# Kernel optimization log

Hardware: AMD Instinct MI355X
Metric: run time of the kernel (lower is better)

The kernel has to match this reference:

```python
import jax, jax.numpy as jnp
import numpy as np

N, E, CS = 8, 256, 8
L2, M2 = 2048, 1024
L1 = M2 * CS            # 8192 tokens at depth-1
M1 = 4096
LLAST = M1 * CS         # 32768 tokens at last layer
S = L2 + L1 + LLAST     # 43008
NUM_VOCAB = 16
RES = 64


def _mixed_values(key, n, L, M):
    # values in {1,3}, with exactly M positions per row set to the 'mixed' token 2
    k1, k2 = jax.random.split(key)
    base = jax.random.randint(k1, (n, L), 0, 2) * 2 + 1
    perms = jax.vmap(lambda k: jax.random.permutation(k, L))(jax.random.split(k2, n))
    mask = jnp.zeros((n, L), bool).at[jnp.arange(n)[:, None], perms[:, :M]].set(True)
    return jnp.where(mask, 2, base).astype(jnp.int32)


def setup_inputs() -> dict:
    key = jax.random.key(0)
    ks = jax.random.split(key, 16)
    v2 = _mixed_values(ks[0], N, L2, M2)
    v1 = _mixed_values(ks[1], N, L1, M1)
    vl = jax.random.randint(ks[2], (N, LLAST), 1, 4).astype(jnp.int32)
    value = jnp.concatenate([v2, v1, vl], axis=1)
    depth = jnp.concatenate([
        jnp.full((N, L2), 4, jnp.int32),
        jnp.full((N, L1), 5, jnp.int32),
        jnp.full((N, LLAST), 6, jnp.int32)], axis=1)
    pos = jax.random.randint(ks[3], (N, S, 3), 0, RES).astype(jnp.int32)
    x = jax.random.normal(ks[4], (N, L2 // CS, E), jnp.float32)
    s = 0.02
    return {
        'x': x, 'value': value, 'depth': depth, 'pos': pos,
        'W2': jax.random.normal(ks[5], (E, E, CS), jnp.float32) * s,
        'b2': jax.random.normal(ks[6], (E,), jnp.float32) * s,
        'W1': jax.random.normal(ks[7], (E, E, CS), jnp.float32) * s,
        'b1': jax.random.normal(ks[8], (E,), jnp.float32) * s,
        'W0': jax.random.normal(ks[9], (E, E, CS), jnp.float32) * s,
        'b0': jax.random.normal(ks[10], (E,), jnp.float32) * s,
        'emb': jax.random.normal(ks[11], (3, RES, E), jnp.float32) * s,
        'lin_w': jax.random.normal(ks[12], (E, NUM_VOCAB + 1), jnp.float32) * s,
        'lin_b': jax.random.normal(ks[13], (NUM_VOCAB + 1,), jnp.float32) * s,
    }


def _deconv(h, W, b):
    # ConvTranspose1d with kernel_size == stride == CS: each input token emits CS outputs
    n, t, e = h.shape
    cs = W.shape[2]
    return jnp.einsum('nti,iok->ntko', h, W).reshape(n, t * cs, e) + b


def _compact(y, mask, M):
    # per-row: rows of y where mask, packed to the front (stable), zero padded to M rows
    T = y.shape[1]
    if mask.shape[1] < T:
        mask = jnp.pad(mask, ((0, 0), (0, T - mask.shape[1])))
    else:
        mask = mask[:, :T]
    order = jnp.argsort(jnp.where(mask, 0, 1), axis=1, stable=True)
    g = jnp.take_along_axis(y, order[:, :M, None], axis=1)
    keep = jnp.arange(M)[None, :] < jnp.sum(mask, axis=1)[:, None]
    return jnp.where(keep[:, :, None], g, 0.0)


def reference(x, value, depth, pos, W2, b2, W1, b1, W0, b0, emb, lin_w, lin_b):
    max_depth = int(jnp.max(depth))
    len_1 = jnp.sum(depth == max_depth - 1, axis=1)
    len_2 = jnp.sum(depth == max_depth - 2, axis=1)
    L1_ = int(jnp.max(len_1)); L2_ = int(jnp.max(len_2))
    j2 = jnp.arange(L2_); j1 = jnp.arange(L1_)
    val_2 = jnp.where(j2[None, :] < len_2[:, None], value[:, :L2_], 0)
    idx1 = jnp.clip(len_2[:, None] + j1[None, :], 0, value.shape[1] - 1)
    val_1 = jnp.where(j1[None, :] < len_1[:, None], jnp.take_along_axis(value, idx1, axis=1), 0)
    mix_1 = jnp.sum(val_1 == 2, axis=1); mix_2 = jnp.sum(val_2 == 2, axis=1)
    M1_ = int(jnp.max(mix_1)); M2_ = int(jnp.max(mix_2))

    y_2 = _deconv(x, W2, b2)                 # [N, T''*cs, E]
    x_1 = _compact(y_2, val_2 == 2, M2_)     # gather mixed depth-2 positions
    y_1 = _deconv(x_1, W1, b1)
    x_0 = _compact(y_1, val_1 == 2, M1_)     # gather mixed depth-1 positions
    y_0 = _deconv(x_0, W0, b0)               # [N, M1_*cs, E]

    len_last = int(jnp.sum(depth[0] == max_depth))  # uniform across batch (torch slicing requires it)
    p = pos[:, -len_last:]                   # [N, len_last, 3]
    enc = emb[0][p[..., 0]] + emb[1][p[..., 1]] + emb[2][p[..., 2]]
    y_0 = y_0 + enc
    return y_0 @ lin_w + lin_b
```

## Files before the change

### kernel.cpp

```cpp
#include <hip/hip_runtime.h>
#include <cstdint>
#include <cstddef>

#define SEQ     43008
#define LASTOFF 10240
#define NV      17

typedef __bf16 bf16x8 __attribute__((ext_vector_type(8)));
typedef float  f32x4  __attribute__((ext_vector_type(4)));

typedef __attribute__((address_space(1))) const void gv_t;
typedef __attribute__((address_space(3))) void       lv_t;

__device__ __forceinline__ ushort f2bf(float f) {
    union { float f; unsigned u; } x; x.f = f;
    unsigned r = x.u + 0x7FFFu + ((x.u >> 16) & 1u);
    return (ushort)(r >> 16);
}
__device__ __forceinline__ float bf2f(ushort h) {
    union { unsigned u; float f; } x; x.u = ((unsigned)h) << 16;
    return x.f;
}

__device__ __forceinline__ void stage_tile_w(char* ldsbase, const ushort* src,
                                             int row0, int k0, int nch, int wv,
                                             int nwv, int lane)
{
    int sub  = lane >> 3;
    int col8 = (lane & 7) ^ sub;
    const ushort* g0 = src + (size_t)(row0 + sub) * 256 + k0 + (col8 << 3);
    for (int ch = wv; ch < nch; ch += nwv) {
        const ushort* g = g0 + ((size_t)(ch << 3)) * 256;
        __builtin_amdgcn_global_load_lds((gv_t*)g, (lv_t*)(ldsbase + (ch << 10)), 16, 0, 0);
    }
}

__device__ __forceinline__ bf16x8 frag64(const char* lds, int row, int kk, int lane) {
    int r = row + (lane & 15);
    int byte = (r << 7) + ((kk + ((lane >> 4) << 3)) << 1);
    byte ^= (r & 7) << 4;
    return *(const bf16x8*)(lds + byte);
}

__global__ __launch_bounds__(256) void prep_main(
    const float* __restrict__ x, const float* __restrict__ W2,
    const float* __restrict__ W1, const float* __restrict__ W0,
    const float* __restrict__ lin_w, const int* __restrict__ value,
    const float* __restrict__ emb, const float* __restrict__ b0,
    const float* __restrict__ lin_b,
    ushort* __restrict__ xb, ushort* __restrict__ WbT,
    ushort* __restrict__ W1n, int* __restrict__ dest2,
    int* __restrict__ packT, int* __restrict__ cnt1,
    float* __restrict__ embLp)
{
    __shared__ __align__(16) char sm[33792];
    const int b = blockIdx.x;
    const int tid = threadIdx.x;

    if (b < 192) {
        int s   = b >> 6;
        int rem = b & 63;
        int i0  = (rem >> 3) << 5;
        int o0  = (rem & 7) << 5;
        const float* W = (s == 0) ? W2 : ((s == 1) ? W1 : W0);
        float* tl = (float*)sm;
        #pragma unroll
        for (int q = 0; q < 8; ++q) {
            int fid = (q << 8) + tid;
            int ri  = fid >> 6;
            int f   = (fid & 63) << 2;
            float4 v = *(const float4*)(W + (size_t)(i0 + ri) * 2048 + o0 * 8 + f);
            int ol = f >> 3;
            int c0 = f & 7;
            tl[((c0 + 0) * 32 + ol) * 33 + ri] = v.x;
            tl[((c0 + 1) * 32 + ol) * 33 + ri] = v.y;
            tl[((c0 + 2) * 32 + ol) * 33 + ri] = v.z;
            tl[((c0 + 3) * 32 + ol) * 33 + ri] = v.w;
        }
        __syncthreads();
        int seg = tid & 3;
        if (s == 1) {
            #pragma unroll
            for (int it = 0; it < 4; ++it) {
                int rk = (it << 6) + (tid >> 2);
                int c = rk >> 5, ii = rk & 31;
                ushort v8[8];
                #pragma unroll
                for (int u = 0; u < 8; ++u)
                    v8[u] = f2bf(tl[(c * 32 + (seg << 3) + u) * 33 + ii]);
                *(int4*)(W1n + (c << 16) + (i0 + ii) * 256 + o0 + (seg << 3)) =
                    *(const int4*)v8;
            }
        } else {
            #pragma unroll
            for (int it = 0; it < 4; ++it) {
                int rk = (it << 6) + (tid >> 2);
                int j  = ((rk >> 5) << 8) + o0 + (rk & 31);
                ushort v8[8];
                #pragma unroll
                for (int u = 0; u < 8; ++u)
                    v8[u] = f2bf(tl[rk * 33 + (seg << 3) + u]);
                *(int4*)(WbT + ((size_t)s << 19) + ((size_t)j << 8) + i0 + (seg << 3)) =
                    *(const int4*)v8;
            }
        }
    } else if (b < 448) {
        int i8 = (((b - 192) << 8) + tid) << 3;
        float4 a  = *(const float4*)(x + i8);
        float4 bb = *(const float4*)(x + i8 + 4);
        ushort v[8] = { f2bf(a.x), f2bf(a.y), f2bf(a.z), f2bf(a.w),
                        f2bf(bb.x), f2bf(bb.y), f2bf(bb.z), f2bf(bb.w) };
        *(int4*)(xb + i8) = *(const int4*)v;
    } else if (b < 456) {
        int n    = b - 448;
        int base = n * SEQ;
        int* dst = dest2 + n * 2048;
        int cnt = 0;
        int vloc[8];
        #pragma unroll
        for (int i = 0; i < 8; ++i) {
            vloc[i] = value[base + tid * 8 + i];
            cnt += (vloc[i] == 2);
        }
        int* s = (int*)sm;
        s[tid] = cnt;
        __syncthreads();
        for (int off = 1; off < 256; off <<= 1) {
            int v = (tid >= off) ? s[tid - off] : 0;
            __syncthreads();
            s[tid] += v;
            __syncthreads();
        }
        int run = s[tid] - cnt;
        #pragma unroll
        for (int i = 0; i < 8; ++i) {
            int d = -1;
            if (vloc[i] == 2 && run < 1024) { d = run; ++run; }
            dst[tid * 8 + i] = d;
        }
    } else if (b < 464) {
        int n    = b - 456;
        int base = n * SEQ + 2048;
        int (*s8)[8] = (int(*)[8])sm;
        int cnt8[8] = {0,0,0,0,0,0,0,0};
        int vloc[32];
        #pragma unroll
        for (int i = 0; i < 32; ++i) {
            vloc[i] = value[base + tid * 32 + i];
            cnt8[i & 7] += (vloc[i] == 2);
        }
        #pragma unroll
        for (int k = 0; k < 8; ++k) s8[tid][k] = cnt8[k];
        __syncthreads();
        for (int off = 1; off < 256; off <<= 1) {
            int v[8];
            #pragma unroll
            for (int k = 0; k < 8; ++k) v[k] = (tid >= off) ? s8[tid - off][k] : 0;
            __syncthreads();
            #pragma unroll
            for (int k = 0; k < 8; ++k) s8[tid][k] += v[k];
            __syncthreads();
        }
        int runK[8], runTot = 0;
        #pragma unroll
        for (int k = 0; k < 8; ++k) { runK[k] = s8[tid][k] - cnt8[k]; runTot += runK[k]; }
        #pragma unroll
        for (int i = 0; i < 32; ++i) {
            if (vloc[i] == 2) {
                int k  = i & 7;
                int tp = (tid * 32 + i) >> 3;
                packT[(((n << 3) + k) << 10) + runK[k]] = (runTot << 16) | tp;
                runK[k]++; runTot++;
            }
        }
        if (tid < 8) cnt1[(n << 3) + tid] = s8[255][tid];
    } else {
        int idx = b - 464;
        int jd  = idx >> 6;
        int p   = idx & 63;
        float* er = (float*)sm;
        float* ps = er + 256;
        float e = emb[jd * 16384 + p * 256 + tid];
        if (jd == 0) e += b0[tid];
        er[tid] = e;
        __syncthreads();
        if (tid < 136) {
            int v = tid >> 3, part = tid & 7;
            const float* lw = lin_w + v;
            float s = 0.f;
            int o0 = part << 5;
            #pragma unroll 8
            for (int o = o0; o < o0 + 32; ++o)
                s = fmaf(er[o], lw[o * NV], s);
            ps[tid] = s;
        }
        __syncthreads();
        if (tid < 20) {
            float acc = 0.f;
            if (tid < NV) {
                #pragma unroll
                for (int q = 0; q < 8; ++q) acc += ps[tid * 8 + q];
                if (jd == 0) acc += lin_b[tid];
            }
            embLp[jd * 1280 + p * 20 + tid] = acc;
        }
    }
}

__global__ __launch_bounds__(256) void prep_g2(
    const ushort* __restrict__ Wb0T, const float* __restrict__ lin_w,
    ushort* __restrict__ Gt,
    const ushort* __restrict__ A, const ushort* __restrict__ BT,
    const float* __restrict__ bias, const int* __restrict__ dest,
    ushort* __restrict__ Xout)
{
    __shared__ __align__(16) char smem[65536];
    const int tid = threadIdx.x;

    if (blockIdx.x < 144) {
        int col = blockIdx.x;
        if (col >= 136) { Gt[col * 256 + tid] = 0; return; }
        int c = (col * 964) >> 14;
        int v = col - c * 17;
        float* lw = (float*)smem;
        lw[tid] = lin_w[tid * NV + v];
        __syncthreads();
        const ushort* wrow = Wb0T + ((size_t)c << 16) + tid;
        float acc = 0.f;
        #pragma unroll 4
        for (int q = 0; q < 256; ++q)
            acc = fmaf(lw[q], bf2f(wrow[q << 8]), acc);
        Gt[col * 256 + tid] = f2bf(acc);
        return;
    }

    const int bx   = blockIdx.x - 144;
    const int lane = tid & 63, wv = tid >> 6;
    const int r0 = (bx & 15) << 7;
    const int c0 = (bx >> 4) << 7;
    const int wm = (wv >> 1) << 6;
    const int wn = (wv & 1) << 6;

    f32x4 acc[4][4] = {};

    stage_tile_w(smem,         A,  r0, 0, 16, wv, 4, lane);
    stage_tile_w(smem + 16384, BT, c0, 0, 16, wv, 4, lane);
    __syncthreads();

    for (int kt = 0; kt < 4; ++kt) {
        char* cb = smem + ((kt & 1) << 15);
        if (kt < 3) {
            char* nb = smem + (((kt + 1) & 1) << 15);
            int k0n = (kt + 1) << 6;
            stage_tile_w(nb,         A,  r0, k0n, 16, wv, 4, lane);
            stage_tile_w(nb + 16384, BT, c0, k0n, 16, wv, 4, lane);
        }
        #pragma unroll
        for (int ks = 0; ks < 2; ++ks) {
            int kk = ks << 5;
            bf16x8 af[4], bfr[4];
            #pragma unroll
            for (int i = 0; i < 4; ++i) af[i]  = frag64(cb, wm + i * 16, kk, lane);
            #pragma unroll
            for (int i = 0; i < 4; ++i) bfr[i] = frag64(cb + 16384, wn + i * 16, kk, lane);
            #pragma unroll
            for (int mi = 0; mi < 4; ++mi)
                #pragma unroll
                for (int ni = 0; ni < 4; ++ni)
                    acc[mi][ni] = __builtin_amdgcn_mfma_f32_16x16x32_bf16(
                        af[mi], bfr[ni], acc[mi][ni], 0, 0, 0);
        }
        __syncthreads();
    }

    const int obase = c0 & 255;
    const int cdx   = c0 >> 8;
    float bv[4];
    #pragma unroll
    for (int ni = 0; ni < 4; ++ni)
        bv[ni] = bias[obase + wn + ni * 16 + (lane & 15)];

    ushort* Cs = (ushort*)smem;
    #pragma unroll
    for (int mi = 0; mi < 4; ++mi)
        #pragma unroll
        for (int ni = 0; ni < 4; ++ni)
            #pragma unroll
            for (int r = 0; r < 4; ++r) {
                int row = wm + mi * 16 + ((lane >> 4) << 2) + r;
                int col = wn + ni * 16 + (lane & 15);
                Cs[row * 136 + col] = f2bf(acc[mi][ni][r] + bv[ni]);
            }
    __syncthreads();

    for (int p = 0; p < 8; ++p) {
        int row = p * 16 + (tid >> 4);
        int gr  = r0 + row;
        int n   = gr >> 8, t = gr & 255;
        int d   = dest[n * 2048 + t * 8 + cdx];
        if (d >= 0) {
            int4 v = *(const int4*)&Cs[row * 136 + ((tid & 15) << 3)];
            *(int4*)&Xout[(((size_t)n * 1024 + d) << 8) + obase + ((tid & 15) << 3)] = v;
        }
    }
}

__global__ __launch_bounds__(256) void prep_H(
    const ushort* __restrict__ Gt, const ushort* __restrict__ W1n,
    const float* __restrict__ b1, ushort* __restrict__ Hf,
    float* __restrict__ K1f)
{
    __shared__ __align__(16) char smem[38912];
    const int tid = threadIdx.x, lane = tid & 63, wv = tid >> 6;
    const int cp = blockIdx.y, fb = blockIdx.x;

    if (cp == 8) {
        if (fb != 0) return;
        float* bs = (float*)smem;
        bs[tid] = b1[tid];
        __syncthreads();
        if (tid < 144) {
            const ushort* gr = Gt + tid * 256;
            float acc = 0.f;
            #pragma unroll 8
            for (int o = 0; o < 256; ++o)
                acc = fmaf(bs[o], bf2f(gr[o]), acc);
            K1f[tid] = acc;
        }
        return;
    }

    const ushort* Wb = W1n + (cp << 16);
    f32x4 acc[3][4] = {};

    for (int kt = 0; kt < 4; ++kt) {
        int k0 = kt << 6;
        stage_tile_w(smem,        Gt, fb * 48, k0, 6,  wv, 4, lane);
        stage_tile_w(smem + 6144, Wb, 0,       k0, 32, wv, 4, lane);
        __syncthreads();
        #pragma unroll
        for (int ks = 0; ks < 2; ++ks) {
            int kk = ks << 5;
            bf16x8 af[3], bfr[4];
            #pragma unroll
            for (int mi = 0; mi < 3; ++mi) af[mi]  = frag64(smem, mi * 16, kk, lane);
            #pragma unroll
            for (int ni = 0; ni < 4; ++ni) bfr[ni] = frag64(smem + 6144, (wv << 6) + ni * 16, kk, lane);
            #pragma unroll
            for (int mi = 0; mi < 3; ++mi)
                #pragma unroll
                for (int ni = 0; ni < 4; ++ni)
                    acc[mi][ni] = __builtin_amdgcn_mfma_f32_16x16x32_bf16(
                        af[mi], bfr[ni], acc[mi][ni], 0, 0, 0);
        }
        __syncthreads();
    }

    #pragma unroll
    for (int mi = 0; mi < 3; ++mi)
        #pragma unroll
        for (int ni = 0; ni < 4; ++ni)
            #pragma unroll
            for (int r = 0; r < 4; ++r) {
                int f = fb * 48 + mi * 16 + ((lane >> 4) << 2) + r;
                int i = (wv << 6) + ni * 16 + (lane & 15);
                Hf[cp * 36864 + f * 256 + i] = f2bf(acc[mi][ni][r]);
            }
}

__global__ __launch_bounds__(256) void fused_out(
    const ushort* __restrict__ X1, const ushort* __restrict__ Hf,
    const float* __restrict__ embLp, const float* __restrict__ K1f,
    const int* __restrict__ packT, const int* __restrict__ cnt1,
    const int* __restrict__ pos, float* __restrict__ out)
{
    extern __shared__ __align__(16) char smem[];

    const int tid  = threadIdx.x;
    const int lane = tid & 63, wv = tid >> 6;
    const int bb = blockIdx.x;
    const int n  = bb >> 3, cp = bb & 7;
    const int t0 = blockIdx.y << 6;
    const int cnt = cnt1[bb];
    if (t0 >= cnt) return;
    const int cntL = min(64, cnt - t0);

    const int sub  = lane >> 3;
    const int col8 = (lane & 7) ^ sub;
    const int* pbase = packT + (bb << 10);
    int Ta = pbase[t0 + (wv << 3) + sub] & 1023;
    int Tb = pbase[t0 + ((wv + 4) << 3) + sub] & 1023;
    const ushort* ga0 = X1 + ((size_t)((n << 10) + Ta) << 8) + (col8 << 3);
    const ushort* gb0 = X1 + ((size_t)((n << 10) + Tb) << 8) + (col8 << 3);

    float* embLs = (float*)(smem + 53248);
    for (int i = tid; i < 3840; i += 256) embLs[i] = embLp[i];
    float* K1s = (float*)(smem + 68608);
    if (tid < 144) K1s[tid] = K1f[tid];
    int* Ds = (int*)(smem + 69184);
    if (tid < 64) Ds[tid] = (pbase[t0 + tid] >> 16) & 4095;

    const ushort* Hb = Hf + cp * 36864;

    __builtin_amdgcn_global_load_lds((gv_t*)ga0, (lv_t*)(smem + (wv << 10)), 16, 0, 0);
    __builtin_amdgcn_global_load_lds((gv_t*)gb0, (lv_t*)(smem + ((wv + 4) << 10)), 16, 0, 0);
    stage_tile_w(smem + 8192, Hb, 0, 0, 18, wv, 4, lane);
    __syncthreads();

    f32x4 acc[9] = {};
    for (int kt = 0; kt < 4; ++kt) {
        char* cb = smem + (kt & 1) * 26624;
        if (kt < 3) {
            char* nb = smem + ((kt + 1) & 1) * 26624;
            int k0n = (kt + 1) << 6;
            __builtin_amdgcn_global_load_lds((gv_t*)(ga0 + k0n), (lv_t*)(nb + (wv << 10)), 16, 0, 0);
            __builtin_amdgcn_global_load_lds((gv_t*)(gb0 + k0n), (lv_t*)(nb + ((wv + 4) << 10)), 16, 0, 0);
            stage_tile_w(nb + 8192, Hb, 0, k0n, 18, wv, 4, lane);
        }
        #pragma unroll
        for (int ks = 0; ks < 2; ++ks) {
            int kk = ks << 5;
            bf16x8 af = frag64(cb, wv << 4, kk, lane);
            #pragma unroll
            for (int ni = 0; ni < 9; ++ni) {
                bf16x8 bfr = frag64(cb + 8192, ni << 4, kk, lane);
                acc[ni] = __builtin_amdgcn_mfma_f32_16x16x32_bf16(af, bfr, acc[ni], 0, 0, 0);
            }
        }
        __syncthreads();
    }

    float* Cs = (float*)smem;
    #pragma unroll
    for (int ni = 0; ni < 9; ++ni) {
        int col = (ni << 4) + (lane & 15);
        if (col < 136) {
            #pragma unroll
            for (int r = 0; r < 4; ++r) {
                int row = (wv << 4) + ((lane >> 4) << 2) + r;
                Cs[row * 136 + col] = acc[ni][r];
            }
        }
    }
    __syncthreads();

    #pragma unroll
    for (int rr = 0; rr < 2; ++rr) {
        int rl = tid * 2 + rr;
        int r  = rl >> 3, c = rl & 7;
        int prow = n * SEQ + LASTOFF + (Ds[r] << 3) + c;
        const int* pp = pos + 3 * prow;
        const float* e0 = embLs +        pp[0] * 20;
        const float* e1 = embLs + 1280 + pp[1] * 20;
        const float* e2 = embLs + 2560 + pp[2] * 20;
        const float* k1 = K1s + c * 17;
        float* cr = Cs + rl * 17;
        #pragma unroll
        for (int v4 = 0; v4 < 16; v4 += 4) {
            float4 a = *(const float4*)(e0 + v4);
            float4 bq = *(const float4*)(e1 + v4);
            float4 cq = *(const float4*)(e2 + v4);
            cr[v4 + 0] += a.x + bq.x + cq.x + k1[v4 + 0];
            cr[v4 + 1] += a.y + bq.y + cq.y + k1[v4 + 1];
            cr[v4 + 2] += a.z + bq.z + cq.z + k1[v4 + 2];
            cr[v4 + 3] += a.w + bq.w + cq.w + k1[v4 + 3];
        }
        cr[16] += e0[16] + e1[16] + e2[16] + k1[16];
    }
    __syncthreads();

    for (int i4 = tid; i4 < 2176; i4 += 256) {
        int r  = (i4 * 1928) >> 16;
        int fo = i4 - r * 34;
        if (r < cntL) {
            *(float4*)(out + ((size_t)((n << 12) + Ds[r])) * 136 + (fo << 2)) =
                *(const float4*)(Cs + r * 136 + (fo << 2));
        }
    }
}

extern "C" void kernel_launch(void* const* d_in, const int* in_sizes, int n_in,
                              void* d_out, int out_size, void* d_ws, size_t ws_size,
                              hipStream_t stream)
{
    (void)in_sizes; (void)n_in; (void)out_size; (void)ws_size;
    const float* x     = (const float*)d_in[0];
    const int*   value = (const int*)d_in[1];
    const int*   pos   = (const int*)d_in[3];
    const float* W2    = (const float*)d_in[4];
    const float* b2    = (const float*)d_in[5];
    const float* W1    = (const float*)d_in[6];
    const float* b1    = (const float*)d_in[7];
    const float* W0    = (const float*)d_in[8];
    const float* b0    = (const float*)d_in[9];
    const float* emb   = (const float*)d_in[10];
    const float* lin_w = (const float*)d_in[11];
    const float* lin_b = (const float*)d_in[12];
    float* out = (float*)d_out;

    char* ws = (char*)d_ws;
    ushort* WbT   = (ushort*)(ws);
    ushort* Wb2T  = WbT;
    ushort* Wb0T  = WbT + 1048576;
    ushort* W1n   = (ushort*)(ws + 3145728);
    ushort* xb    = (ushort*)(ws + 4194304);
    int*    dest2 = (int*)   (ws + 5242880);
    int*    cnt1  = (int*)   (ws + 5308416);
    int*    packT = (int*)   (ws + 5308672);
    ushort* x1b   = (ushort*)(ws + 5570816);
    ushort* Gt    = (ushort*)(ws + 9765120);
    float*  embLp = (float*) (ws + 9838848);
    ushort* Hf    = (ushort*)(ws + 9854208);
    float*  K1f   = (float*) (ws + 10444032);

    prep_main<<<656, 256, 0, stream>>>(x, W2, W1, W0, lin_w, value,
                                       emb, b0, lin_b,
                                       xb, WbT, W1n, dest2, packT, cnt1, embLp);
    prep_g2<<<400, 256, 0, stream>>>(Wb0T, lin_w, Gt, xb, Wb2T, b2, dest2, x1b);
    prep_H<<<dim3(3, 9), 256, 0, stream>>>(Gt, W1n, b1, Hf, K1f);

    fused_out<<<dim3(64, 16), 256, 69632, stream>>>(x1b, Hf, embLp, K1f,
                                                    packT, cnt1, pos, out);
}
```

Baseline: 62.88 us.

## Fuse Gt and H precomputation into the depth-2 deconv kernel

Merges prep_g2 and prep_H into one kernel g2h. Its first 256 blocks run the depth-2 GEMM and scatter, and 64 extra blocks each compute the Gt slice (W0 folded with lin_w) for one channel group and then run the H GEMM against W1 straight from shared memory. K1f is computed by a reduction in the cp==0 blocks. This removes one kernel launch and the Gt round trip through global memory. In exchange, each (cp,cf) block recomputes its Gt slice redundantly, eight times in total, and the small blocks may form a tail behind the large GEMM blocks.

```diff
diff --git a/kernel.cpp b/kernel.cpp
--- a/kernel.cpp
+++ b/kernel.cpp
@@ -207,165 +207,182 @@
     }
 }
 
-__global__ __launch_bounds__(256) void prep_g2(
-    const ushort* __restrict__ Wb0T, const float* __restrict__ lin_w,
-    ushort* __restrict__ Gt,
+__global__ __launch_bounds__(256) void g2h(
     const ushort* __restrict__ A, const ushort* __restrict__ BT,
     const float* __restrict__ bias, const int* __restrict__ dest,
-    ushort* __restrict__ Xout)
+    ushort* __restrict__ Xout,
+    const ushort* __restrict__ Wb0T, const float* __restrict__ lin_w,
+    const ushort* __restrict__ W1n, const float* __restrict__ b1,
+    ushort* __restrict__ Hf, float* __restrict__ K1f)
 {
-    __shared__ __align__(16) char smem[65536];
+    extern __shared__ __align__(16) char smem[];
     const int tid = threadIdx.x;
 
-    if (blockIdx.x < 144) {
-        int col = blockIdx.x;
-        if (col >= 136) { Gt[col * 256 + tid] = 0; return; }
-        int c = (col * 964) >> 14;
-        int v = col - c * 17;
-        float* lw = (float*)smem;
-        lw[tid] = lin_w[tid * NV + v];
-        __syncthreads();
-        const ushort* wrow = Wb0T + ((size_t)c << 16) + tid;
-        float acc = 0.f;
-        #pragma unroll 4
-        for (int q = 0; q < 256; ++q)
-            acc = fmaf(lw[q], bf2f(wrow[q << 8]), acc);
-        Gt[col * 256 + tid] = f2bf(acc);
+    if (blockIdx.x < 256) {
+        const int lane = tid & 63, wv = tid >> 6;
+        const int bx = blockIdx.x;
+        const int r0 = (bx & 15) << 7;
+        const int c0 = (bx >> 4) << 7;
+        const int wm = (wv >> 1) << 6;
+        const int wn = (wv & 1) << 6;
+
+        f32x4 acc[4][4] = {};
+
+        stage_tile_w(smem,         A,  r0, 0, 16, wv, 4, lane);
+        stage_tile_w(smem + 16384, BT, c0, 0, 16, wv, 4, lane);
+        __syncthreads();
+
+        for (int kt = 0; kt < 4; ++kt) {
+            char* cb = smem + ((kt & 1) << 15);
+            if (kt < 3) {
+                char* nb = smem + (((kt + 1) & 1) << 15);
+                int k0n = (kt + 1) << 6;
+                stage_tile_w(nb,         A,  r0, k0n, 16, wv, 4, lane);
+                stage_tile_w(nb + 16384, BT, c0, k0n, 16, wv, 4, lane);
+            }
+            #pragma unroll
+            for (int ks = 0; ks < 2; ++ks) {
+                int kk = ks << 5;
+                bf16x8 af[4], bfr[4];
+                #pragma unroll
+                for (int i = 0; i < 4; ++i) af[i]  = frag64(cb, wm + i * 16, kk, lane);
+                #pragma unroll
+                for (int i = 0; i < 4; ++i) bfr[i] = frag64(cb + 16384, wn + i * 16, kk, lane);
+                #pragma unroll
+                for (int mi = 0; mi < 4; ++mi)
+                    #pragma unroll
+                    for (int ni = 0; ni < 4; ++ni)
+                        acc[mi][ni] = __builtin_amdgcn_mfma_f32_16x16x32_bf16(
+                            af[mi], bfr[ni], acc[mi][ni], 0, 0, 0);
+            }
+            __syncthreads();
+        }
+
+        const int obase = c0 & 255;
+        const int cdx   = c0 >> 8;
+        float bv[4];
+        #pragma unroll
+        for (int ni = 0; ni < 4; ++ni)
+            bv[ni] = bias[obase + wn + ni * 16 + (lane & 15)];
+
+        ushort* Cs = (ushort*)smem;
+        #pragma unroll
+        for (int mi = 0; mi < 4; ++mi)
+            #pragma unroll
+            for (int ni = 0; ni < 4; ++ni)
+                #pragma unroll
+                for (int r = 0; r < 4; ++r) {
+                    int row = wm + mi * 16 + ((lane >> 4) << 2) + r;
+                    int col = wn + ni * 16 + (lane & 15);
+                    Cs[row * 136 + col] = f2bf(acc[mi][ni][r] + bv[ni]);
+                }
+        __syncthreads();
+
+        for (int p = 0; p < 8; ++p) {
+            int row = p * 16 + (tid >> 4);
+            int gr  = r0 + row;
+            int n   = gr >> 8, t = gr & 255;
+            int d   = dest[n * 2048 + t * 8 + cdx];
+            if (d >= 0) {
+                int4 v = *(const int4*)&Cs[row * 136 + ((tid & 15) << 3)];
+                *(int4*)&Xout[(((size_t)n * 1024 + d) << 8) + obase + ((tid & 15) << 3)] = v;
+            }
+        }
         return;
     }
 
-    const int bx   = blockIdx.x - 144;
+    const int idx = blockIdx.x - 256;
+    const int cp  = idx >> 3, cf = idx & 7;
     const int lane = tid & 63, wv = tid >> 6;
-    const int r0 = (bx & 15) << 7;
-    const int c0 = (bx >> 4) << 7;
-    const int wm = (wv >> 1) << 6;
-    const int wn = (wv & 1) << 6;
-
-    f32x4 acc[4][4] = {};
-
-    stage_tile_w(smem,         A,  r0, 0, 16, wv, 4, lane);
-    stage_tile_w(smem + 16384, BT, c0, 0, 16, wv, 4, lane);
-    __syncthreads();
-
+
+    float* lwS = (float*)smem;
+    float* b1S = (float*)(smem + 17408);
+    for (int j = tid; j < 4352; j += 256) {
+        int v = j >> 8, q = j & 255;
+        lwS[j] = lin_w[q * NV + v];
+    }
+    b1S[tid] = b1[tid];
+    __syncthreads();
+
+    float gv[17];
+    #pragma unroll
+    for (int v = 0; v < 17; ++v) gv[v] = 0.f;
+    const ushort* wb = Wb0T + ((size_t)cf << 16) + tid;
+    for (int q = 0; q < 256; ++q) {
+        float w = bf2f(wb[q << 8]);
+        #pragma unroll
+        for (int v = 0; v < 17; ++v)
+            gv[v] = fmaf(w, lwS[(v << 8) + q], gv[v]);
+    }
+
+    float* Kr = (float*)(smem + 20480);
+    {
+        float bo = b1S[tid];
+        #pragma unroll
+        for (int v = 0; v < 17; ++v) Kr[(v << 8) + tid] = gv[v] * bo;
+    }
+    __syncthreads();
+    if (cp == 0) {
+        for (int s = 128; s >= 1; s >>= 1) {
+            for (int v = 0; v < 17; ++v)
+                if (tid < s) Kr[(v << 8) + tid] += Kr[(v << 8) + tid + s];
+            __syncthreads();
+        }
+        if (tid < 17) K1f[cf * 17 + tid] = Kr[tid << 8];
+        if (cf == 7 && tid >= 136 && tid < 144) K1f[tid] = 0.f;
+    }
+    __syncthreads();
+
+    ushort* Gs = (ushort*)smem;
+    for (int j = tid; j < 4096; j += 256) ((int*)Gs)[j] = 0;
+    __syncthreads();
+    {
+        int kt = tid >> 6, kloc = tid & 63;
+        #pragma unroll
+        for (int v = 0; v < 17; ++v) {
+            int byte = (v << 7) + (kloc << 1);
+            byte ^= (v & 7) << 4;
+            *(ushort*)((char*)Gs + (kt << 12) + byte) = f2bf(gv[v]);
+        }
+    }
+    __syncthreads();
+
+    char* Bs = smem + 16384;
+    const ushort* Wb1 = W1n + ((size_t)cp << 16);
+    f32x4 hacc[2][16] = {};
     for (int kt = 0; kt < 4; ++kt) {
-        char* cb = smem + ((kt & 1) << 15);
-        if (kt < 3) {
-            char* nb = smem + (((kt + 1) & 1) << 15);
-            int k0n = (kt + 1) << 6;
-            stage_tile_w(nb,         A,  r0, k0n, 16, wv, 4, lane);
-            stage_tile_w(nb + 16384, BT, c0, k0n, 16, wv, 4, lane);
-        }
+        stage_tile_w(Bs, Wb1, 0, kt << 6, 32, wv, 4, lane);
+        __syncthreads();
         #pragma unroll
         for (int ks = 0; ks < 2; ++ks) {
             int kk = ks << 5;
-            bf16x8 af[4], bfr[4];
-            #pragma unroll
-            for (int i = 0; i < 4; ++i) af[i]  = frag64(cb, wm + i * 16, kk, lane);
-            #pragma unroll
-            for (int i = 0; i < 4; ++i) bfr[i] = frag64(cb + 16384, wn + i * 16, kk, lane);
-            #pragma unroll
-            for (int mi = 0; mi < 4; ++mi)
-                #pragma unroll
-                for (int ni = 0; ni < 4; ++ni)
-                    acc[mi][ni] = __builtin_amdgcn_mfma_f32_16x16x32_bf16(
-                        af[mi], bfr[ni], acc[mi][ni], 0, 0, 0);
-        }
-        __syncthreads();
-    }
-
-    const int obase = c0 & 255;
-    const int cdx   = c0 >> 8;
-    float bv[4];
+            bf16x8 af0 = frag64((char*)Gs + (kt << 12), 0,  kk, lane);
+            bf16x8 af1 = frag64((char*)Gs + (kt << 12), 16, kk, lane);
+            #pragma unroll
+            for (int ni = 0; ni < 16; ++ni) {
+                bf16x8 bfr = frag64(Bs, ni << 4, kk, lane);
+                hacc[0][ni] = __builtin_amdgcn_mfma_f32_16x16x32_bf16(af0, bfr, hacc[0][ni], 0, 0, 0);
+                hacc[1][ni] = __builtin_amdgcn_mfma_f32_16x16x32_bf16(af1, bfr, hacc[1][ni], 0, 0, 0);
+            }
+        }
+        __syncthreads();
+    }
+
     #pragma unroll
-    for (int ni = 0; ni < 4; ++ni)
-        bv[ni] = bias[obase + wn + ni * 16 + (lane & 15)];
-
-    ushort* Cs = (ushort*)smem;
-    #pragma unroll
-    for (int mi = 0; mi < 4; ++mi)
-        #pragma unroll
-        for (int ni = 0; ni < 4; ++ni)
+    for (int mi = 0; mi < 2; ++mi)
+        #pragma unroll
+        for (int ni = 0; ni < 16; ++ni)
             #pragma unroll
             for (int r = 0; r < 4; ++r) {
-                int row = wm + mi * 16 + ((lane >> 4) << 2) + r;
-                int col = wn + ni * 16 + (lane & 15);
-                Cs[row * 136 + col] = f2bf(acc[mi][ni][r] + bv[ni]);
-            }
-    __syncthreads();
-
-    for (int p = 0; p < 8; ++p) {
-        int row = p * 16 + (tid >> 4);
-        int gr  = r0 + row;
-        int n   = gr >> 8, t = gr & 255;
-        int d   = dest[n * 2048 + t * 8 + cdx];
-        if (d >= 0) {
-            int4 v = *(const int4*)&Cs[row * 136 + ((tid & 15) << 3)];
-            *(int4*)&Xout[(((size_t)n * 1024 + d) << 8) + obase + ((tid & 15) << 3)] = v;
-        }
-    }
-}
-
-__global__ __launch_bounds__(256) void prep_H(
-    const ushort* __restrict__ Gt, const ushort* __restrict__ W1n,
-    const float* __restrict__ b1, ushort* __restrict__ Hf,
-    float* __restrict__ K1f)
-{
-    __shared__ __align__(16) char smem[38912];
-    const int tid = threadIdx.x, lane = tid & 63, wv = tid >> 6;
-    const int cp = blockIdx.y, fb = blockIdx.x;
-
-    if (cp == 8) {
-        if (fb != 0) return;
-        float* bs = (float*)smem;
-        bs[tid] = b1[tid];
-        __syncthreads();
-        if (tid < 144) {
-            const ushort* gr = Gt + tid * 256;
-            float acc = 0.f;
-            #pragma unroll 8
-            for (int o = 0; o < 256; ++o)
-                acc = fmaf(bs[o], bf2f(gr[o]), acc);
-            K1f[tid] = acc;
-        }
-        return;
-    }
-
-    const ushort* Wb = W1n + (cp << 16);
-    f32x4 acc[3][4] = {};
-
-    for (int kt = 0; kt < 4; ++kt) {
-        int k0 = kt << 6;
-        stage_tile_w(smem,        Gt, fb * 48, k0, 6,  wv, 4, lane);
-        stage_tile_w(smem + 6144, Wb, 0,       k0, 32, wv, 4, lane);
-        __syncthreads();
-        #pragma unroll
-        for (int ks = 0; ks < 2; ++ks) {
-            int kk = ks << 5;
-            bf16x8 af[3], bfr[4];
-            #pragma unroll
-            for (int mi = 0; mi < 3; ++mi) af[mi]  = frag64(smem, mi * 16, kk, lane);
-            #pragma unroll
-            for (int ni = 0; ni < 4; ++ni) bfr[ni] = frag64(smem + 6144, (wv << 6) + ni * 16, kk, lane);
-            #pragma unroll
-            for (int mi = 0; mi < 3; ++mi)
-                #pragma unroll
-                for (int ni = 0; ni < 4; ++ni)
-                    acc[mi][ni] = __builtin_amdgcn_mfma_f32_16x16x32_bf16(
-                        af[mi], bfr[ni], acc[mi][ni], 0, 0, 0);
-        }
-        __syncthreads();
-    }
-
-    #pragma unroll
-    for (int mi = 0; mi < 3; ++mi)
-        #pragma unroll
-        for (int ni = 0; ni < 4; ++ni)
-            #pragma unroll
-            for (int r = 0; r < 4; ++r) {
-                int f = fb * 48 + mi * 16 + ((lane >> 4) << 2) + r;
-                int i = (wv << 6) + ni * 16 + (lane & 15);
-                Hf[cp * 36864 + f * 256 + i] = f2bf(acc[mi][ni][r]);
-            }
+                int v = (mi << 4) + ((lane >> 4) << 2) + r;
+                if (v < 17) {
+                    int i = (ni << 4) + (lane & 15);
+                    Hf[cp * 36864 + (cf * 17 + v) * 256 + i] = f2bf(hacc[mi][ni][r]);
+                }
+            }
+    if (cf == 7)
+        for (int j = tid; j < 2048; j += 256)
+            Hf[cp * 36864 + 136 * 256 + j] = 0;
 }
 
 __global__ __launch_bounds__(256) void fused_out(
@@ -508,7 +525,6 @@
     int*    cnt1  = (int*)   (ws + 5308416);
     int*    packT = (int*)   (ws + 5308672);
     ushort* x1b   = (ushort*)(ws + 5570816);
-    ushort* Gt    = (ushort*)(ws + 9765120);
     float*  embLp = (float*) (ws + 9838848);
     ushort* Hf    = (ushort*)(ws + 9854208);
     float*  K1f   = (float*) (ws + 10444032);
@@ -516,9 +532,8 @@
     prep_main<<<656, 256, 0, stream>>>(x, W2, W1, W0, lin_w, value,
                                        emb, b0, lin_b,
                                        xb, WbT, W1n, dest2, packT, cnt1, embLp);
-    prep_g2<<<400, 256, 0, stream>>>(Wb0T, lin_w, Gt, xb, Wb2T, b2, dest2, x1b);
-    prep_H<<<dim3(3, 9), 256, 0, stream>>>(Gt, W1n, b1, Hf, K1f);
-
+    g2h<<<320, 256, 65536, stream>>>(xb, Wb2T, b2, dest2, x1b,
+                                     Wb0T, lin_w, W1n, b1, Hf, K1f);
     fused_out<<<dim3(64, 16), 256, 69632, stream>>>(x1b, Hf, embLp, K1f,
                                                     packT, cnt1, pos, out);
 }
```

New measurement: 77.26 us. +22.9%, slower.
